# Kernel tuning notes

Measured on AMD Instinct MI355X. Metric: run time of the kernel, lower is better.

The kernel has to match this reference:

```python
import jax, jax.numpy as jnp
import numpy as np
import math

INC, OUTC, N, STRIDE = 128, 256, 9, 1
B, H, W = 8, 64, 64
EPS = 1e-5


def setup_inputs() -> dict:
    key = jax.random.key(0)
    k0, k1, k2, k3 = jax.random.split(key, 4)
    x = jax.random.normal(k0, (B, INC, H, W), jnp.float32)
    # p_conv: 3x3 conv inc -> 2N (torch inits weight=0; use small random so offsets are nontrivial)
    pw = jax.random.normal(k1, (2 * N, INC, 3, 3), jnp.float32) * 0.01
    pb = jax.random.normal(k2, (2 * N,), jnp.float32) * 0.01
    # final 1x1 conv inc -> outc (bias=None in the module), BN affine params
    cw = jax.random.normal(k3, (OUTC, INC, 1, 1), jnp.float32) * (1.0 / math.sqrt(INC))
    gamma = jnp.ones((OUTC,), jnp.float32)
    beta = jnp.zeros((OUTC,), jnp.float32)
    return dict(x=x, pw=pw, pb=pb, cw=cw, gamma=gamma, beta=beta)


def _akconv(x, pw, pb, cw, gamma, beta):
    b, c, Hx, Wx = x.shape
    # offset = p_conv(x): 3x3 conv, padding 1, stride STRIDE -> (b, 2N, h, w)
    offset = jax.lax.conv_general_dilated(
        x, pw, window_strides=(STRIDE, STRIDE), padding=((1, 1), (1, 1)),
        dimension_numbers=("NCHW", "OIHW", "NCHW")) + pb[None, :, None, None]
    h, w = offset.shape[2], offset.shape[3]

    # p_n: N points on unit circle (x=cos, y=sin), concat -> (2N,)
    angles = jnp.linspace(0.0, 2.0 * math.pi, N + 1)[:-1]
    p_n = jnp.concatenate([jnp.cos(angles), jnp.sin(angles)])  # (2N,)

    # p_0: base grid positions, (2N, h, w)
    gx = jnp.broadcast_to((jnp.arange(h, dtype=jnp.float32) * STRIDE)[:, None], (h, w))
    gy = jnp.broadcast_to((jnp.arange(w, dtype=jnp.float32) * STRIDE)[None, :], (h, w))
    p0 = jnp.concatenate([jnp.broadcast_to(gx[None], (N, h, w)),
                          jnp.broadcast_to(gy[None], (N, h, w))], axis=0)

    p = (offset + p_n[None, :, None, None] + p0[None]).transpose(0, 2, 3, 1)  # (b,h,w,2N)
    px, py = p[..., :N], p[..., N:]

    fx = jnp.floor(jax.lax.stop_gradient(px))  # q is detached in the original
    fy = jnp.floor(jax.lax.stop_gradient(py))
    q_ltx = jnp.clip(fx, 0, Hx - 1)
    q_lty = jnp.clip(fy, 0, Wx - 1)
    q_rbx = jnp.clip(fx + 1.0, 0, Hx - 1)
    q_rby = jnp.clip(fy + 1.0, 0, Wx - 1)
    pxc = jnp.clip(px, 0, Hx - 1)
    pyc = jnp.clip(py, 0, Wx - 1)

    g_lt = (1.0 + (q_ltx - pxc)) * (1.0 + (q_lty - pyc))
    g_rb = (1.0 - (q_rbx - pxc)) * (1.0 - (q_rby - pyc))
    g_lb = (1.0 + (q_ltx - pxc)) * (1.0 - (q_rby - pyc))
    g_rt = (1.0 - (q_rbx - pxc)) * (1.0 + (q_lty - pyc))

    x_flat = x.reshape(b, c, Hx * Wx)

    def gather(qx, qy):
        idx = (qx * Wx + qy).astype(jnp.int32).reshape(b, -1)  # (b, h*w*N)
        xg = jax.vmap(lambda xf, ix: xf[:, ix])(x_flat, idx)    # (b, c, h*w*N)
        return xg.reshape(b, c, h, w, N)

    x_off = (g_lt[:, None] * gather(q_ltx, q_lty)
             + g_rb[:, None] * gather(q_rbx, q_rby)
             + g_lb[:, None] * gather(q_ltx, q_rby)
             + g_rt[:, None] * gather(q_rbx, q_lty))  # (b,c,h,w,N)

    x_off = x_off.reshape(b, c, h, w * N)  # 'b c h w n -> b c h (w n)'

    # 1x1 conv (no bias) + BatchNorm (training-mode batch stats) + SiLU
    y = jnp.einsum("bchw,oc->bohw", x_off, cw[:, :, 0, 0])
    mean = jnp.mean(y, axis=(0, 2, 3), keepdims=True)
    var = jnp.var(y, axis=(0, 2, 3), keepdims=True)
    yn = (y - mean) * jax.lax.rsqrt(var + EPS)
    yn = yn * gamma[None, :, None, None] + beta[None, :, None, None]
    return yn * jax.nn.sigmoid(yn)


def reference(x, pw, pb, cw, gamma, beta):
    return _akconv(x, pw, pb, cw, gamma, beta)
```

## Files before the change

### kernel.cpp

```cpp
#include <hip/hip_runtime.h>
#include <math.h>

#define INC   128
#define OUTC  256
#define NPTS  9
#define BATCH 8
#define HDIM  64
#define WDIM  64
#define HW    4096
#define JLB   36864
#define JTOT  294912
#define NTOTF 294912.0f

typedef __bf16 bf16x8 __attribute__((ext_vector_type(8)));
typedef __bf16 bf16x4 __attribute__((ext_vector_type(4)));
typedef float  f32x4  __attribute__((ext_vector_type(4)));

__global__ void k_cvt_cw(const float* __restrict__ cw, __bf16* __restrict__ cwb) {
    int i = blockIdx.x * 256 + threadIdx.x;
    if (i < OUTC * INC) cwb[i] = (__bf16)cw[i];
}

__global__ __launch_bounds__(256) void k_transpose(
        const float* __restrict__ x, __bf16* __restrict__ xTb) {
    __shared__ __bf16 t[64 * 128];
    char* tb = (char*)t;
    int b   = blockIdx.x >> 6;
    int hw0 = (blockIdx.x & 63) << 6;
    int tid = threadIdx.x;
    int lane = tid & 63;
    int cq  = tid >> 6;
    const float* xb = x + b * (INC * HW);
    #pragma unroll
    for (int cc = 0; cc < INC; cc += 4) {
        int c = cc + cq;
        float v = xb[c * HW + hw0 + lane];
        *(__bf16*)(tb + lane * 256 + ((2 * c) ^ ((lane & 15) << 4))) = (__bf16)v;
    }
    __syncthreads();
    __bf16* ob = xTb + ((size_t)b * HW + hw0) * INC;
    #pragma unroll
    for (int i = 0; i < 4; ++i) {
        int chunk = i * 256 + tid;
        int hw  = chunk >> 4;
        int c16 = chunk & 15;
        bf16x8 vv = *(bf16x8*)(tb + hw * 256 + ((c16 * 16) ^ ((hw & 15) << 4)));
        *(bf16x8*)(ob + hw * INC + c16 * 8) = vv;
    }
}

__global__ __launch_bounds__(256) void k_prep(
        const float* __restrict__ x, const float* __restrict__ pw,
        const float* __restrict__ pb, int4* __restrict__ sidx,
        float4* __restrict__ sw) {
    int n  = blockIdx.x >> 7;
    int sp = ((blockIdx.x & 127) << 8) + threadIdx.x;
    int b  = sp >> 12;
    int hh = (sp >> 6) & 63;
    int ww = sp & 63;

    __shared__ float pwl[INC * 9 * 2];
    for (int i = threadIdx.x; i < INC * 9; i += 256) {
        pwl[i * 2 + 0] = pw[n * (INC * 9) + i];
        pwl[i * 2 + 1] = pw[(n + 9) * (INC * 9) + i];
    }
    __syncthreads();

    const float* xb = x + b * (INC * HW);
    float ax = 0.f, ay = 0.f;
    for (int c = 0; c < INC; ++c) {
        const float* xc = xb + c * HW;
        const float* pc = pwl + c * 18;
        #pragma unroll
        for (int ky = 0; ky < 3; ++ky) {
            int yy = hh - 1 + ky;
            #pragma unroll
            for (int kx = 0; kx < 3; ++kx) {
                int xx = ww - 1 + kx;
                float v = ((unsigned)yy < 64u && (unsigned)xx < 64u)
                            ? xc[yy * 64 + xx] : 0.f;
                int k = ky * 3 + kx;
                ax = fmaf(v, pc[k * 2 + 0], ax);
                ay = fmaf(v, pc[k * 2 + 1], ay);
            }
        }
    }
    ax += pb[n];
    ay += pb[n + 9];

    const float TWO_PI = 6.28318530717958647692f;
    float ang = (float)n * (TWO_PI / 9.0f);
    float px = ax + cosf(ang) + (float)hh;
    float py = ay + sinf(ang) + (float)ww;
    float fx = floorf(px), fy = floorf(py);
    float ltx = fminf(fmaxf(fx,        0.f), 63.f);
    float lty = fminf(fmaxf(fy,        0.f), 63.f);
    float rbx = fminf(fmaxf(fx + 1.f,  0.f), 63.f);
    float rby = fminf(fmaxf(fy + 1.f,  0.f), 63.f);
    float pxc = fminf(fmaxf(px,        0.f), 63.f);
    float pyc = fminf(fmaxf(py,        0.f), 63.f);
    float glt = (1.f + ltx - pxc) * (1.f + lty - pyc);
    float grb = (1.f - rbx + pxc) * (1.f - rby + pyc);
    float glb = (1.f + ltx - pxc) * (1.f - rby + pyc);
    float grt = (1.f - rbx + pxc) * (1.f + lty - pyc);

    int j = b * JLB + (hh * 64 + ww) * 9 + n;
    sidx[j] = make_int4((int)ltx * 64 + (int)lty,
                        (int)rbx * 64 + (int)rby,
                        (int)ltx * 64 + (int)rby,
                        (int)rbx * 64 + (int)lty);
    sw[j] = make_float4(glt, grb, glb, grt);
}

__device__ __forceinline__ void gather_tile(
        const __bf16* __restrict__ xTb, const int4* __restrict__ sidx,
        const float4* __restrict__ sw, int b, int jl0, int tid, char* xoffT) {
    int col = tid >> 2;
    int q   = tid & 3;
    int j   = b * JLB + jl0 + col;
    int4   qi = sidx[j];
    float4 qw = sw[j];
    const __bf16* xtb = xTb + (size_t)b * (HW * INC) + q * 32;

    float accc[32];
    #pragma unroll
    for (int i = 0; i < 32; ++i) accc[i] = 0.f;

    const int   idx4[4] = { qi.x, qi.y, qi.z, qi.w };
    const float wt4[4]  = { qw.x, qw.y, qw.z, qw.w };
    #pragma unroll
    for (int p = 0; p < 4; ++p) {
        const __bf16* rp = xtb + idx4[p] * INC;
        float wp = wt4[p];
        #pragma unroll
        for (int v = 0; v < 4; ++v) {
            bf16x8 vv = *(const bf16x8*)(rp + v * 8);
            #pragma unroll
            for (int i = 0; i < 8; ++i)
                accc[v * 8 + i] = fmaf(wp, (float)vv[i], accc[v * 8 + i]);
        }
    }
    #pragma unroll
    for (int i8 = 0; i8 < 4; ++i8) {
        bf16x8 pk;
        #pragma unroll
        for (int i = 0; i < 8; ++i) pk[i] = (__bf16)accc[i8 * 8 + i];
        int colbyte = (q * 64 + i8 * 16) ^ ((col & 7) << 4);
        *(bf16x8*)(xoffT + col * 256 + colbyte) = pk;
    }
}

__global__ __launch_bounds__(256, 2) void k_gemm_fused(
        const __bf16* __restrict__ xTb, const __bf16* __restrict__ cwb,
        const int4* __restrict__ sidx, const float4* __restrict__ sw,
        float* __restrict__ gstat, __bf16* __restrict__ yb) {
    __shared__ uint4 xoffT4[64 * 256 / 16];
    __shared__ float saux[512];
    char* xoffT = (char*)xoffT4;

    int bidx = blockIdx.x;
    int b    = bidx / 576;
    int jl0  = (bidx % 576) * 64;
    int tid  = threadIdx.x;
    int w    = tid >> 6;
    int l    = tid & 63;

    gather_tile(xTb, sidx, sw, b, jl0, tid, xoffT);

    bf16x8 bfrag[4][4];
    #pragma unroll
    for (int ot = 0; ot < 4; ++ot) {
        int o = w * 64 + ot * 16 + (l & 15);
        #pragma unroll
        for (int ks = 0; ks < 4; ++ks) {
            int k = ks * 32 + (l >> 4) * 8;
            bfrag[ot][ks] = *(const bf16x8*)(cwb + o * 128 + k);
        }
    }
    __syncthreads();

    f32x4 acc[4][4] = {};
    #pragma unroll
    for (int ks = 0; ks < 4; ++ks) {
        bf16x8 afrag[4];
        #pragma unroll
        for (int jt = 0; jt < 4; ++jt) {
            int row = jt * 16 + (l & 15);
            int colbyte = (ks * 64 + (l >> 4) * 16) ^ ((row & 7) << 4);
            afrag[jt] = *(const bf16x8*)(xoffT + row * 256 + colbyte);
        }
        #pragma unroll
        for (int jt = 0; jt < 4; ++jt)
            #pragma unroll
            for (int ot = 0; ot < 4; ++ot)
                acc[jt][ot] = __builtin_amdgcn_mfma_f32_16x16x32_bf16(
                    afrag[jt], bfrag[ot][ks], acc[jt][ot], 0, 0, 0);
    }

    __bf16* ybb = yb + (size_t)b * (OUTC * JLB);
    #pragma unroll
    for (int ot = 0; ot < 4; ++ot) {
        int o = w * 64 + ot * 16 + (l & 15);
        __bf16* yrow = ybb + (size_t)o * JLB + jl0 + (l >> 4) * 4;
        #pragma unroll
        for (int jt = 0; jt < 4; ++jt) {
            bf16x4 pk;
            #pragma unroll
            for (int r = 0; r < 4; ++r) pk[r] = (__bf16)acc[jt][ot][r];
            *(bf16x4*)(yrow + jt * 16) = pk;
        }
    }

    float* ssum = saux;
    float* ssq  = saux + 256;
    #pragma unroll
    for (int ot = 0; ot < 4; ++ot) {
        float s = 0.f, qq = 0.f;
        #pragma unroll
        for (int jt = 0; jt < 4; ++jt)
            #pragma unroll
            for (int r = 0; r < 4; ++r) {
                float v = acc[jt][ot][r];
                s  += v;
                qq += v * v;
            }
        s  += __shfl_xor(s, 16);
        s  += __shfl_xor(s, 32);
        qq += __shfl_xor(qq, 16);
        qq += __shfl_xor(qq, 32);
        if (l < 16) {
            int o = w * 64 + ot * 16 + l;
            ssum[o] = s;
            ssq[o]  = qq;
        }
    }
    __syncthreads();
    float* gs = gstat + (bidx & 63) * 512;
    atomicAdd(gs + tid,       ssum[tid]);
    atomicAdd(gs + 256 + tid, ssq[tid]);
}

__global__ __launch_bounds__(256) void k_norm(
        const __bf16* __restrict__ yb, const float* __restrict__ scaleb,
        const float* __restrict__ shiftb, float* __restrict__ out) {
    int base = blockIdx.x * 2048;
    #pragma unroll
    for (int it = 0; it < 8; ++it) {
        int chunk = base + it * 256 + threadIdx.x;
        int row = (unsigned)chunk / 4608u;
        int o   = row & 255;
        float sc = scaleb[o];
        float sh = shiftb[o];
        bf16x8 v = *(const bf16x8*)(yb + (size_t)chunk * 8);
        f32x4 r0, r1;
        #pragma unroll
        for (int k = 0; k < 4; ++k) {
            float yn = fmaf((float)v[k], sc, sh);
            r0[k] = yn / (1.f + __expf(-yn));
        }
        #pragma unroll
        for (int k = 0; k < 4; ++k) {
            float yn = fmaf((float)v[4 + k], sc, sh);
            r1[k] = yn / (1.f + __expf(-yn));
        }
        float* op = out + (size_t)chunk * 8;
        *(f32x4*)op       = r0;
        *(f32x4*)(op + 4) = r1;
    }
}

template <bool WRITE>
__global__ __launch_bounds__(256, 2) void k_gemm(
        const __bf16* __restrict__ xTb, const __bf16* __restrict__ cwb,
        const int4* __restrict__ sidx, const float4* __restrict__ sw,
        const float* __restrict__ scaleb, const float* __restrict__ shiftb,
        float* __restrict__ gstat, float* __restrict__ out) {
    __shared__ uint4 xoffT4[64 * 256 / 16];
    __shared__ float saux[512];
    char* xoffT = (char*)xoffT4;

    int bidx = blockIdx.x;
    int b    = bidx / 576;
    int jl0  = (bidx % 576) * 64;
    int tid  = threadIdx.x;
    int w    = tid >> 6;
    int l    = tid & 63;

    gather_tile(xTb, sidx, sw, b, jl0, tid, xoffT);

    if (WRITE) {
        saux[tid]       = scaleb[tid];
        saux[256 + tid] = shiftb[tid];
        bf16x8 bfrag[4][4];
        #pragma unroll
        for (int ot = 0; ot < 4; ++ot) {
            int o = w * 64 + ot * 16 + (l & 15);
            #pragma unroll
            for (int ks = 0; ks < 4; ++ks) {
                int k = ks * 32 + (l >> 4) * 8;
                bfrag[ot][ks] = *(const bf16x8*)(cwb + o * 128 + k);
            }
        }
        __syncthreads();

        f32x4 acc[4][4] = {};
        #pragma unroll
        for (int ks = 0; ks < 4; ++ks) {
            bf16x8 afrag[4];
            #pragma unroll
            for (int jt = 0; jt < 4; ++jt) {
                int row = jt * 16 + (l & 15);
                int colbyte = (ks * 64 + (l >> 4) * 16) ^ ((row & 7) << 4);
                afrag[jt] = *(const bf16x8*)(xoffT + row * 256 + colbyte);
            }
            #pragma unroll
            for (int jt = 0; jt < 4; ++jt)
                #pragma unroll
                for (int ot = 0; ot < 4; ++ot)
                    acc[jt][ot] = __builtin_amdgcn_mfma_f32_16x16x32_bf16(
                        afrag[jt], bfrag[ot][ks], acc[jt][ot], 0, 0, 0);
        }

        float* outb = out + (size_t)b * (OUTC * JLB);
        #pragma unroll
        for (int ot = 0; ot < 4; ++ot) {
            int o = w * 64 + ot * 16 + (l & 15);
            float sc = saux[o];
            float sh = saux[256 + o];
            float* orow = outb + (size_t)o * JLB + jl0 + (l >> 4) * 4;
            #pragma unroll
            for (int jt = 0; jt < 4; ++jt) {
                f32x4 vst;
                #pragma unroll
                for (int r = 0; r < 4; ++r) {
                    float yn = fmaf(acc[jt][ot][r], sc, sh);
                    vst[r] = yn / (1.f + __expf(-yn));
                }
                *(f32x4*)(orow + jt * 16) = vst;
            }
        }
    } else {
        bf16x8 afrag[4][4];
        #pragma unroll
        for (int mt = 0; mt < 4; ++mt) {
            int m = w * 64 + mt * 16 + (l & 15);
            #pragma unroll
            for (int ks = 0; ks < 4; ++ks) {
                int k = ks * 32 + (l >> 4) * 8;
                afrag[mt][ks] = *(const bf16x8*)(cwb + m * 128 + k);
            }
        }
        __syncthreads();

        f32x4 acc[4][4] = {};
        #pragma unroll
        for (int ks = 0; ks < 4; ++ks) {
            bf16x8 bfrag[4];
            #pragma unroll
            for (int nt = 0; nt < 4; ++nt) {
                int row = nt * 16 + (l & 15);
                int colbyte = (ks * 64 + (l >> 4) * 16) ^ ((row & 7) << 4);
                bfrag[nt] = *(const bf16x8*)(xoffT + row * 256 + colbyte);
            }
            #pragma unroll
            for (int mt = 0; mt < 4; ++mt)
                #pragma unroll
                for (int nt = 0; nt < 4; ++nt)
                    acc[mt][nt] = __builtin_amdgcn_mfma_f32_16x16x32_bf16(
                        afrag[mt][ks], bfrag[nt], acc[mt][nt], 0, 0, 0);
        }

        float* ssum = saux;
        float* ssq  = saux + 256;
        #pragma unroll
        for (int mt = 0; mt < 4; ++mt) {
            #pragma unroll
            for (int r = 0; r < 4; ++r) {
                float s = 0.f, qq = 0.f;
                #pragma unroll
                for (int nt = 0; nt < 4; ++nt) {
                    float v = acc[mt][nt][r];
                    s  += v;
                    qq += v * v;
                }
                #pragma unroll
                for (int d = 1; d < 16; d <<= 1) {
                    s  += __shfl_xor(s, d, 64);
                    qq += __shfl_xor(qq, d, 64);
                }
                if ((l & 15) == 0) {
                    int row = w * 64 + mt * 16 + (l >> 4) * 4 + r;
                    ssum[row] = s;
                    ssq[row]  = qq;
                }
            }
        }
        __syncthreads();
        float* gs = gstat + (bidx & 63) * 512;
        atomicAdd(gs + tid,       ssum[tid]);
        atomicAdd(gs + 256 + tid, ssq[tid]);
    }
}

__global__ void k_stats(const float* __restrict__ gstat,
                        const float* __restrict__ gamma,
                        const float* __restrict__ beta,
                        float* __restrict__ scaleb, float* __restrict__ shiftb) {
    int t = threadIdx.x;
    float s = 0.f, q = 0.f;
    for (int r = 0; r < 64; ++r) {
        s += gstat[r * 512 + t];
        q += gstat[r * 512 + 256 + t];
    }
    float mean = s / NTOTF;
    float var  = q / NTOTF - mean * mean;
    float rstd = rsqrtf(var + 1e-5f);
    float sc = rstd * gamma[t];
    scaleb[t] = sc;
    shiftb[t] = beta[t] - mean * sc;
}

extern "C" void kernel_launch(void* const* d_in, const int* in_sizes, int n_in,
                              void* d_out, int out_size, void* d_ws, size_t ws_size,
                              hipStream_t stream) {
    (void)in_sizes; (void)n_in; (void)out_size;
    const float* x     = (const float*)d_in[0];
    const float* pw    = (const float*)d_in[1];
    const float* pb    = (const float*)d_in[2];
    const float* cw    = (const float*)d_in[3];
    const float* gamma = (const float*)d_in[4];
    const float* beta  = (const float*)d_in[5];
    float* out = (float*)d_out;

    char* ws = (char*)d_ws;
    const size_t Y_BYTES = (size_t)JTOT * OUTC * 2;
    bool big = ws_size >= (Y_BYTES + 18087936ull);

    size_t off = big ? Y_BYTES : 0;
    __bf16* yb    = (__bf16*)ws;
    __bf16* xTb   = (__bf16*)(ws + off);
    int4*   sidx  = (int4*)(ws + off + 8388608);
    float4* swt   = (float4*)(ws + off + 13107200);
    __bf16* cwb   = (__bf16*)(ws + off + 17825792);
    float*  gstat = (float*)(ws + off + 17891328);
    float*  scaleb= (float*)(ws + off + 18022400);
    float*  shiftb= (float*)(ws + off + 18023424);

    hipMemsetAsync(gstat, 0, 64 * 512 * 4, stream);
    k_cvt_cw<<<128, 256, 0, stream>>>(cw, cwb);
    k_transpose<<<512, 256, 0, stream>>>(x, xTb);
    k_prep<<<9 * 128, 256, 0, stream>>>(x, pw, pb, sidx, swt);
    if (big) {
        k_gemm_fused<<<4608, 256, 0, stream>>>(xTb, cwb, sidx, swt, gstat, yb);
        k_stats<<<1, 256, 0, stream>>>(gstat, gamma, beta, scaleb, shiftb);
        k_norm<<<4608, 256, 0, stream>>>(yb, scaleb, shiftb, out);
    } else {
        k_gemm<false><<<4608, 256, 0, stream>>>(xTb, cwb, sidx, swt,
                                                nullptr, nullptr, gstat, nullptr);
        k_stats<<<1, 256, 0, stream>>>(gstat, gamma, beta, scaleb, shiftb);
        k_gemm<true><<<4608, 256, 0, stream>>>(xTb, cwb, sidx, swt,
                                               scaleb, shiftb, gstat, out);
    }
}
```

Before: 270.5 us.

## Materialize gathered bf16 tiles once and recompute GEMM instead of storing y

The fused gather+GEMM kernel that wrote a bf16 y buffer (about 150MB) followed by a normalize pass is replaced by three stages. A gather kernel writes pre-swizzled bf16 x_off tiles (about 75MB), a stats GEMM streams them into LDS via global_load_lds, and an output GEMM recomputes y and applies BN and SiLU directly in its epilogue. This trades an extra GEMM pass and an extra launch for less HBM traffic, since it avoids the large y write and read-back. The stats GEMM also swaps the operand roles, reducing along rows with 16-lane shuffles.

```diff
diff --git a/kernel.cpp b/kernel.cpp
--- a/kernel.cpp
+++ b/kernel.cpp
@@ -13,8 +13,13 @@
 #define NTOTF 294912.0f
 
 typedef __bf16 bf16x8 __attribute__((ext_vector_type(8)));
-typedef __bf16 bf16x4 __attribute__((ext_vector_type(4)));
 typedef float  f32x4  __attribute__((ext_vector_type(4)));
+
+__device__ __forceinline__ void load_lds16(const void* g, void* lds) {
+    __builtin_amdgcn_global_load_lds(
+        (const __attribute__((address_space(1))) unsigned int*)g,
+        (__attribute__((address_space(3))) unsigned int*)lds, 16, 0, 0);
+}
 
 __global__ void k_cvt_cw(const float* __restrict__ cw, __bf16* __restrict__ cwb) {
     int i = blockIdx.x * 256 + threadIdx.x;
@@ -112,9 +117,10 @@
     sw[j] = make_float4(glt, grb, glb, grt);
 }
 
-__device__ __forceinline__ void gather_tile(
+__device__ __forceinline__ void gather_pack(
         const __bf16* __restrict__ xTb, const int4* __restrict__ sidx,
-        const float4* __restrict__ sw, int b, int jl0, int tid, char* xoffT) {
+        const float4* __restrict__ sw, int b, int jl0, int tid,
+        bf16x8 pk[4], int offs[4]) {
     int col = tid >> 2;
     int q   = tid & 3;
     int j   = b * JLB + jl0 + col;
@@ -142,18 +148,110 @@
     }
     #pragma unroll
     for (int i8 = 0; i8 < 4; ++i8) {
-        bf16x8 pk;
-        #pragma unroll
-        for (int i = 0; i < 8; ++i) pk[i] = (__bf16)accc[i8 * 8 + i];
-        int colbyte = (q * 64 + i8 * 16) ^ ((col & 7) << 4);
-        *(bf16x8*)(xoffT + col * 256 + colbyte) = pk;
-    }
-}
-
-__global__ __launch_bounds__(256, 2) void k_gemm_fused(
-        const __bf16* __restrict__ xTb, const __bf16* __restrict__ cwb,
-        const int4* __restrict__ sidx, const float4* __restrict__ sw,
-        float* __restrict__ gstat, __bf16* __restrict__ yb) {
+        #pragma unroll
+        for (int i = 0; i < 8; ++i) pk[i8][i] = (__bf16)accc[i8 * 8 + i];
+        offs[i8] = col * 256 + ((q * 64 + i8 * 16) ^ ((col & 7) << 4));
+    }
+}
+
+__global__ __launch_bounds__(256) void k_gather(
+        const __bf16* __restrict__ xTb, const int4* __restrict__ sidx,
+        const float4* __restrict__ sw, __bf16* __restrict__ xoffG) {
+    int bidx = blockIdx.x;
+    int b    = bidx / 576;
+    int jl0  = (bidx % 576) * 64;
+    bf16x8 pk[4];
+    int offs[4];
+    gather_pack(xTb, sidx, sw, b, jl0, threadIdx.x, pk, offs);
+    char* xg = (char*)xoffG + (size_t)bidx * 16384;
+    #pragma unroll
+    for (int i8 = 0; i8 < 4; ++i8)
+        *(bf16x8*)(xg + offs[i8]) = pk[i8];
+}
+
+__global__ __launch_bounds__(256, 2) void k_statsgemm(
+        const __bf16* __restrict__ xoffG, const __bf16* __restrict__ cwb,
+        float* __restrict__ gstat) {
+    __shared__ uint4 xoffT4[64 * 256 / 16];
+    __shared__ float saux[512];
+    char* xoffT = (char*)xoffT4;
+
+    int bidx = blockIdx.x;
+    int tid  = threadIdx.x;
+    int w    = tid >> 6;
+    int l    = tid & 63;
+
+    const char* gsrc = (const char*)xoffG + (size_t)bidx * 16384 + w * 4096;
+    char*       ldst = xoffT + w * 4096;
+    #pragma unroll
+    for (int it = 0; it < 4; ++it)
+        load_lds16(gsrc + it * 1024 + l * 16, ldst + it * 1024);
+
+    bf16x8 afrag[4][4];
+    #pragma unroll
+    for (int mt = 0; mt < 4; ++mt) {
+        int m = w * 64 + mt * 16 + (l & 15);
+        #pragma unroll
+        for (int ks = 0; ks < 4; ++ks) {
+            int k = ks * 32 + (l >> 4) * 8;
+            afrag[mt][ks] = *(const bf16x8*)(cwb + m * 128 + k);
+        }
+    }
+    __syncthreads();
+
+    f32x4 acc[4][4] = {};
+    #pragma unroll
+    for (int ks = 0; ks < 4; ++ks) {
+        bf16x8 bfrag[4];
+        #pragma unroll
+        for (int nt = 0; nt < 4; ++nt) {
+            int row = nt * 16 + (l & 15);
+            int colbyte = (ks * 64 + (l >> 4) * 16) ^ ((row & 7) << 4);
+            bfrag[nt] = *(const bf16x8*)(xoffT + row * 256 + colbyte);
+        }
+        #pragma unroll
+        for (int mt = 0; mt < 4; ++mt)
+            #pragma unroll
+            for (int nt = 0; nt < 4; ++nt)
+                acc[mt][nt] = __builtin_amdgcn_mfma_f32_16x16x32_bf16(
+                    afrag[mt][ks], bfrag[nt], acc[mt][nt], 0, 0, 0);
+    }
+
+    float* ssum = saux;
+    float* ssq  = saux + 256;
+    #pragma unroll
+    for (int mt = 0; mt < 4; ++mt) {
+        #pragma unroll
+        for (int r = 0; r < 4; ++r) {
+            float s = 0.f, qq = 0.f;
+            #pragma unroll
+            for (int nt = 0; nt < 4; ++nt) {
+                float v = acc[mt][nt][r];
+                s  += v;
+                qq += v * v;
+            }
+            #pragma unroll
+            for (int d = 1; d < 16; d <<= 1) {
+                s  += __shfl_xor(s, d, 64);
+                qq += __shfl_xor(qq, d, 64);
+            }
+            if ((l & 15) == 0) {
+                int row = w * 64 + mt * 16 + (l >> 4) * 4 + r;
+                ssum[row] = s;
+                ssq[row]  = qq;
+            }
+        }
+    }
+    __syncthreads();
+    float* gs = gstat + (bidx & 63) * 512;
+    atomicAdd(gs + tid,       ssum[tid]);
+    atomicAdd(gs + 256 + tid, ssq[tid]);
+}
+
+__global__ __launch_bounds__(256, 2) void k_out2(
+        const __bf16* __restrict__ xoffG, const __bf16* __restrict__ cwb,
+        const float* __restrict__ scaleb, const float* __restrict__ shiftb,
+        float* __restrict__ out) {
     __shared__ uint4 xoffT4[64 * 256 / 16];
     __shared__ float saux[512];
     char* xoffT = (char*)xoffT4;
@@ -165,7 +263,14 @@
     int w    = tid >> 6;
     int l    = tid & 63;
 
-    gather_tile(xTb, sidx, sw, b, jl0, tid, xoffT);
+    const char* gsrc = (const char*)xoffG + (size_t)bidx * 16384 + w * 4096;
+    char*       ldst = xoffT + w * 4096;
+    #pragma unroll
+    for (int it = 0; it < 4; ++it)
+        load_lds16(gsrc + it * 1024 + l * 16, ldst + it * 1024);
+
+    saux[tid]       = scaleb[tid];
+    saux[256 + tid] = shiftb[tid];
 
     bf16x8 bfrag[4][4];
     #pragma unroll
@@ -197,76 +302,35 @@
                     afrag[jt], bfrag[ot][ks], acc[jt][ot], 0, 0, 0);
     }
 
-    __bf16* ybb = yb + (size_t)b * (OUTC * JLB);
+    float* outb = out + (size_t)b * (OUTC * JLB);
     #pragma unroll
     for (int ot = 0; ot < 4; ++ot) {
         int o = w * 64 + ot * 16 + (l & 15);
-        __bf16* yrow = ybb + (size_t)o * JLB + jl0 + (l >> 4) * 4;
+        float sc = saux[o];
+        float sh = saux[256 + o];
+        float* orow = outb + (size_t)o * JLB + jl0 + (l >> 4) * 4;
         #pragma unroll
         for (int jt = 0; jt < 4; ++jt) {
-            bf16x4 pk;
-            #pragma unroll
-            for (int r = 0; r < 4; ++r) pk[r] = (__bf16)acc[jt][ot][r];
-            *(bf16x4*)(yrow + jt * 16) = pk;
-        }
-    }
-
-    float* ssum = saux;
-    float* ssq  = saux + 256;
-    #pragma unroll
-    for (int ot = 0; ot < 4; ++ot) {
-        float s = 0.f, qq = 0.f;
-        #pragma unroll
-        for (int jt = 0; jt < 4; ++jt)
+            f32x4 vst;
             #pragma unroll
             for (int r = 0; r < 4; ++r) {
-                float v = acc[jt][ot][r];
-                s  += v;
-                qq += v * v;
-            }
-        s  += __shfl_xor(s, 16);
-        s  += __shfl_xor(s, 32);
-        qq += __shfl_xor(qq, 16);
-        qq += __shfl_xor(qq, 32);
-        if (l < 16) {
-            int o = w * 64 + ot * 16 + l;
-            ssum[o] = s;
-            ssq[o]  = qq;
-        }
-    }
-    __syncthreads();
-    float* gs = gstat + (bidx & 63) * 512;
-    atomicAdd(gs + tid,       ssum[tid]);
-    atomicAdd(gs + 256 + tid, ssq[tid]);
-}
-
-__global__ __launch_bounds__(256) void k_norm(
-        const __bf16* __restrict__ yb, const float* __restrict__ scaleb,
-        const float* __restrict__ shiftb, float* __restrict__ out) {
-    int base = blockIdx.x * 2048;
-    #pragma unroll
-    for (int it = 0; it < 8; ++it) {
-        int chunk = base + it * 256 + threadIdx.x;
-        int row = (unsigned)chunk / 4608u;
-        int o   = row & 255;
-        float sc = scaleb[o];
-        float sh = shiftb[o];
-        bf16x8 v = *(const bf16x8*)(yb + (size_t)chunk * 8);
-        f32x4 r0, r1;
-        #pragma unroll
-        for (int k = 0; k < 4; ++k) {
-            float yn = fmaf((float)v[k], sc, sh);
-            r0[k] = yn / (1.f + __expf(-yn));
-        }
-        #pragma unroll
-        for (int k = 0; k < 4; ++k) {
-            float yn = fmaf((float)v[4 + k], sc, sh);
-            r1[k] = yn / (1.f + __expf(-yn));
-        }
-        float* op = out + (size_t)chunk * 8;
-        *(f32x4*)op       = r0;
-        *(f32x4*)(op + 4) = r1;
-    }
+                float yn = fmaf(acc[jt][ot][r], sc, sh);
+                vst[r] = yn / (1.f + __expf(-yn));
+            }
+            *(f32x4*)(orow + jt * 16) = vst;
+        }
+    }
+}
+
+__device__ __forceinline__ void gather_tile(
+        const __bf16* __restrict__ xTb, const int4* __restrict__ sidx,
+        const float4* __restrict__ sw, int b, int jl0, int tid, char* xoffT) {
+    bf16x8 pk[4];
+    int offs[4];
+    gather_pack(xTb, sidx, sw, b, jl0, tid, pk, offs);
+    #pragma unroll
+    for (int i8 = 0; i8 < 4; ++i8)
+        *(bf16x8*)(xoffT + offs[i8]) = pk[i8];
 }
 
 template <bool WRITE>
@@ -433,11 +497,11 @@
     float* out = (float*)d_out;
 
     char* ws = (char*)d_ws;
-    const size_t Y_BYTES = (size_t)JTOT * OUTC * 2;
-    bool big = ws_size >= (Y_BYTES + 18087936ull);
-
-    size_t off = big ? Y_BYTES : 0;
-    __bf16* yb    = (__bf16*)ws;
+    const size_t XOFF_BYTES = (size_t)4608 * 16384;
+    bool big = ws_size >= (XOFF_BYTES + 18087936ull);
+
+    size_t off = big ? XOFF_BYTES : 0;
+    __bf16* xoffG = (__bf16*)ws;
     __bf16* xTb   = (__bf16*)(ws + off);
     int4*   sidx  = (int4*)(ws + off + 8388608);
     float4* swt   = (float4*)(ws + off + 13107200);
@@ -451,9 +515,10 @@
     k_transpose<<<512, 256, 0, stream>>>(x, xTb);
     k_prep<<<9 * 128, 256, 0, stream>>>(x, pw, pb, sidx, swt);
     if (big) {
-        k_gemm_fused<<<4608, 256, 0, stream>>>(xTb, cwb, sidx, swt, gstat, yb);
+        k_gather<<<4608, 256, 0, stream>>>(xTb, sidx, swt, xoffG);
+        k_statsgemm<<<4608, 256, 0, stream>>>(xoffG, cwb, gstat);
         k_stats<<<1, 256, 0, stream>>>(gstat, gamma, beta, scaleb, shiftb);
-        k_norm<<<4608, 256, 0, stream>>>(yb, scaleb, shiftb, out);
+        k_out2<<<4608, 256, 0, stream>>>(xoffG, cwb, scaleb, shiftb, out);
     } else {
         k_gemm<false><<<4608, 256, 0, stream>>>(xTb, cwb, sidx, swt,
                                                 nullptr, nullptr, gstat, nullptr);
```

New measurement: 263.8 us. -2.5%, faster.
